# Performance work log

Measured on AMD Instinct MI355X. Metric: run time of the kernel, lower is better.

## Reference

```python
import jax, jax.numpy as jnp
import numpy as np
import math

B, C, H, W = 64, 32, 80, 80
HEADS, HD = 8, 4
L = H * W
INV_PI = 1.0 / math.pi


def _conv2d(x, w, pad):
    return jax.lax.conv_general_dilated(x, w, (1, 1), pad, dimension_numbers=('NCHW', 'OIHW', 'NCHW'))


def _lin_angular(x, qkv_w, proj_w, proj_b, dconv_w):
    # x: (B, L, C) -> softmax-free angular linear attention
    qkv = (x @ qkv_w.T).reshape(B, L, 3, HEADS, HD).transpose(2, 0, 3, 1, 4)
    q, k, v = qkv[0], qkv[1], qkv[2]  # (B, HEADS, L, HD)
    q = q / jnp.linalg.norm(q, axis=-1, keepdims=True)
    k = k / jnp.linalg.norm(k, axis=-1, keepdims=True)
    # depthwise conv over L with kernel (9,1), one channel per head
    dconv_v = jax.lax.conv_general_dilated(v, dconv_w, (1, 1), ((4, 4), (0, 0)),
                                           feature_group_count=HEADS,
                                           dimension_numbers=('NCHW', 'OIHW', 'NCHW'))
    attn = jnp.einsum('bhld,bhle->bhde', k, v)  # (B,H,HD,HD)
    out = 0.5 * v + INV_PI * jnp.einsum('bhld,bhde->bhle', q, attn)
    out = out / jnp.linalg.norm(out, axis=-1, keepdims=True)
    out = out + dconv_v
    out = out.transpose(0, 2, 1, 3).reshape(B, L, C)
    return out @ proj_w.T + proj_b


def _xca(x, qkv_w, temp, proj_w, proj_b):
    # x: (B, L, C) -> cross-covariance (channel) attention
    qkv = (x @ qkv_w.T).reshape(B, L, 3, HEADS, HD).transpose(2, 0, 3, 4, 1)
    q, k, v = qkv[0], qkv[1], qkv[2]  # (B, HEADS, HD, L)
    q = q / jnp.maximum(jnp.linalg.norm(q, axis=-1, keepdims=True), 1e-12)
    k = k / jnp.maximum(jnp.linalg.norm(k, axis=-1, keepdims=True), 1e-12)
    attn = jax.nn.softmax(jnp.einsum('bhdn,bhen->bhde', q, k) * temp, axis=-1)
    out = jnp.einsum('bhde,bhen->bhdn', attn, v)  # (B,H,HD,L)
    out = out.transpose(0, 3, 1, 2).reshape(B, L, C)
    return out @ proj_w.T + proj_b


def _chan_vec(f, wa, ba, wa2, ba2, wm, bm, wm2, bm2):
    # f: (B, C, L) -> (B, C, 1) pooled channel descriptor (avg + max branches)
    avg = f.mean(axis=-1)  # (B, C)
    mx = f.max(axis=-1)    # (B, C)
    a = jax.nn.relu(avg @ wa.T + ba) @ wa2.T + ba2
    m = jax.nn.relu(mx @ wm.T + bm) @ wm2.T + bm2
    return (a + m)[..., None]  # (B, C, 1)


def _spatial_gate(a, c1w, c1b, c2w, c2b):
    # a: (B, C, L) -> (B, 1, L) softmax spatial gate
    am = a.reshape(B, C, H, W)
    pooled = jnp.concatenate([am.mean(axis=1, keepdims=True), am.max(axis=1, keepdims=True)], axis=1)
    y = jax.nn.relu(_conv2d(pooled, c1w, ((1, 1), (1, 1))) + c1b[None, :, None, None])
    y = _conv2d(y, c2w, ((1, 1), (1, 1))) + c2b[None, :, None, None]
    return jax.nn.softmax(y.reshape(B, 1, L), axis=-1)


def _forward(rgb, freq, la_qkv_w, la_proj_w, la_proj_b, la_dconv_w,
             xa_qkv_w, xa_temp, xa_proj_w, xa_proj_b,
             c1s_w, c1s_b, c2s_w, c2s_b,
             avg1_w, avg1_b, max1_w, max1_b, avg2_w, avg2_b, max2_w, max2_b,
             avg11_w, avg11_b, max11_w, max11_b, avg22_w, avg22_b, max22_w, max22_b):
    x1 = rgb.reshape(B, C, L).transpose(0, 2, 1)  # to_3d: (B, L, C)
    la1 = _lin_angular(x1, la_qkv_w, la_proj_w, la_proj_b, la_dconv_w)
    x2 = freq.reshape(B, C, L).transpose(0, 2, 1)
    xa1 = _xca(x2, xa_qkv_w, xa_temp, xa_proj_w, xa_proj_b)
    # CAFM works on flattened (B, C, L)
    f1 = la1.transpose(0, 2, 1)
    f2 = xa1.transpose(0, 2, 1)
    a1 = _chan_vec(f1, avg1_w, avg1_b, avg11_w, avg11_b, max1_w, max1_b, max11_w, max11_b)
    a2 = _chan_vec(f2, avg2_w, avg2_b, avg22_w, avg22_b, max2_w, max2_b, max22_w, max22_b)
    cross = jnp.einsum('bci,bdi->bcd', a1, a2)  # (B, C, C)
    a1f = jnp.einsum('bcd,bdl->bcl', jax.nn.softmax(cross, axis=-1), f1)
    a2f = jnp.einsum('bcd,bdl->bcl', jax.nn.softmax(cross.transpose(0, 2, 1), axis=-1), f2)
    g1 = _spatial_gate(a1f, c1s_w, c1s_b, c2s_w, c2s_b)
    g2 = _spatial_gate(a2f, c1s_w, c1s_b, c2s_w, c2s_b)
    f1 = f1 * g1 + f1
    f2 = f2 * g2 + f2
    # torch: (B,C,L).transpose(0,1) -> (C,B,L); sum; permute(1,2,0) -> (B,L,C); to_4d -> (B,C,H,W)
    # transposes cancel: equivalent to (f1+f2).reshape(B, C, H, W)
    return (f1 + f2).reshape(B, C, H, W)


def setup_inputs() -> dict:
    key = jax.random.key(0)
    ks = iter(jax.random.split(key, 40))
    def rn(shape, s=0.05):
        return jax.random.normal(next(ks), shape, dtype=jnp.float32) * s
    return dict(
        rgb=jax.random.normal(next(ks), (B, C, H, W), dtype=jnp.float32),
        freq=jax.random.normal(next(ks), (B, C, H, W), dtype=jnp.float32),
        la_qkv_w=rn((3 * C, C)), la_proj_w=rn((C, C)), la_proj_b=jnp.zeros((C,), jnp.float32),
        la_dconv_w=rn((HEADS, 1, 9, 1)),
        xa_qkv_w=rn((3 * C, C)), xa_temp=jnp.ones((HEADS, 1, 1), jnp.float32),
        xa_proj_w=rn((C, C)), xa_proj_b=jnp.zeros((C,), jnp.float32),
        c1s_w=rn((1, 2, 3, 3)), c1s_b=jnp.zeros((1,), jnp.float32),
        c2s_w=rn((1, 1, 3, 3)), c2s_b=jnp.zeros((1,), jnp.float32),
        avg1_w=rn((16, C)), avg1_b=jnp.zeros((16,), jnp.float32),
        max1_w=rn((16, C)), max1_b=jnp.zeros((16,), jnp.float32),
        avg2_w=rn((16, C)), avg2_b=jnp.zeros((16,), jnp.float32),
        max2_w=rn((16, C)), max2_b=jnp.zeros((16,), jnp.float32),
        avg11_w=rn((C, 16)), avg11_b=jnp.zeros((C,), jnp.float32),
        max11_w=rn((C, 16)), max11_b=jnp.zeros((C,), jnp.float32),
        avg22_w=rn((C, 16)), avg22_b=jnp.zeros((C,), jnp.float32),
        max22_w=rn((C, 16)), max22_b=jnp.zeros((C,), jnp.float32),
    )


def reference(rgb, freq, la_qkv_w, la_proj_w, la_proj_b, la_dconv_w,
              xa_qkv_w, xa_temp, xa_proj_w, xa_proj_b,
              c1s_w, c1s_b, c2s_w, c2s_b,
              avg1_w, avg1_b, max1_w, max1_b, avg2_w, avg2_b, max2_w, max2_b,
              avg11_w, avg11_b, max11_w, max11_b, avg22_w, avg22_b, max22_w, max22_b):
    return _forward(rgb, freq, la_qkv_w, la_proj_w, la_proj_b, la_dconv_w,
                    xa_qkv_w, xa_temp, xa_proj_w, xa_proj_b,
                    c1s_w, c1s_b, c2s_w, c2s_b,
                    avg1_w, avg1_b, max1_w, max1_b, avg2_w, avg2_b, max2_w, max2_b,
                    avg11_w, avg11_b, max11_w, max11_b, avg22_w, avg22_b, max22_w, max22_b)
```

## Files before the change

kernel.cpp:

```cpp
#include <hip/hip_runtime.h>

#define BN 64
#define CN 32
#define HEADSN 8
#define HDN 4
#define LN 6400
#define CL (CN*LN)


__device__ __forceinline__ unsigned fenc(float f){
  unsigned u = __float_as_uint(f);
  return (u & 0x80000000u) ? ~u : (u | 0x80000000u);
}
__device__ __forceinline__ float fdec(unsigned u){
  unsigned v = (u & 0x80000000u) ? (u & 0x7FFFFFFFu) : ~u;
  return __uint_as_float(v);
}

__device__ __forceinline__ unsigned pk_bf16(float a, float b){
  unsigned ua = __float_as_uint(a), ub = __float_as_uint(b);
  ua = (ua + 0x7fffu + ((ua >> 16) & 1u)) >> 16;
  ub = (ub + 0x7fffu + ((ub >> 16) & 1u)) >> 16;
  return ua | (ub << 16);
}
// ... 163 lines not shown
    if (lane < 32) atomicAdd(la_attn + b*128 + wave*32 + ch, s);
  } else {
    const float* Wq = Wxa + (0  + wave*8)*32;
    const float* Wk = Wxa + (32 + wave*8)*32;
    float acc[48];
    #pragma unroll
    for (int i = 0; i < 48; ++i) acc[i] = 0.f;
    for (int it = 0; it < 2; ++it){
      const int ll = it*64 + lane;
      float xv[32];
      #pragma unroll
      for (int c2 = 0; c2 < 16; ++c2){
        float2 t = xs[ll*17 + c2];
        xv[2*c2] = t.x; xv[2*c2+1] = t.y;
      }
      float qq[8], kk[8];
      #pragma unroll
      for (int r = 0; r < 8; ++r){ qq[r] = 0.f; kk[r] = 0.f; }
      #pragma unroll
      for (int c = 0; c < 32; ++c){
        #pragma unroll
        for (int r = 0; r < 8; ++r){
          qq[r] = fmaf(Wq[r*32 + c], xv[c], qq[r]);
          kk[r] = fmaf(Wk[r*32 + c], xv[c], kk[r]);
        }
      }
      #pragma unroll
      for (int hh = 0; hh < 2; ++hh){
        const float* q = qq + hh*4;
        const float* k = kk + hh*4;
        const int base = hh*24;
        #pragma unroll
        for (int d = 0; d < 4; ++d){
          #pragma unroll
          for (int e = 0; e < 4; ++e)
            acc[base + d*4 + e] = fmaf(q[d], k[e], acc[base + d*4 + e]);
        }
        #pragma unroll
        for (int d = 0; d < 4; ++d) acc[base + 16 + d] = fmaf(q[d], q[d], acc[base + 16 + d]);
        #pragma unroll
        for (int e = 0; e < 4; ++e) acc[base + 20 + e] = fmaf(k[e], k[e], acc[base + 20 + e]);
      }
    }
    float* dst = xa_sums + b*192 + wave*48;
    int ch;
    float s0 = bfly32<false>(acc, lane, &ch);
    if (lane < 32) atomicAdd(dst + ch, s0);
    int ch2;
    float s1 = bfly16_sum(acc + 32, lane, &ch2);
    if (lane < 16) atomicAdd(dst + 32 + ch2, s1);
  }
}

__global__ __launch_bounds__(512) void k_finalize2(const float* __restrict__ rgb,
    const float* __restrict__ freq, const float* __restrict__ Wqkv,
    const float* __restrict__ la_attn, const float* __restrict__ dconv_w,
    const float* __restrict__ Wp, const float* __restrict__ bp,
    const float* __restrict__ Wxa, const float* __restrict__ xtemp,
    const float* __restrict__ xWp, const float* __restrict__ xbp,
    const float* __restrict__ xa_sums,
    float* __restrict__ f1, float* __restrict__ sum1, unsigned* __restrict__ max1e,
    float* __restrict__ f2, float* __restrict__ sum2, unsigned* __restrict__ max2e){
  __shared__ unsigned vsh[2*264*17];
  const bool isXA = blockIdx.x >= 13;
  const int b = blockIdx.y, tid = threadIdx.x;
  const int half = tid >> 8, t = tid & 255;
  const int bxt = isXA ? (int)blockIdx.x - 13 : (int)blockIdx.x;
  const int tile = bxt*2 + half;
  const bool valid = tile < 25;
  const int l0 = tile*256;
  const int l = l0 + t, lane = tid & 63;
  unsigned* vs = vsh + half*(264*17);
  if (!isXA){
    const float* xg = rgb + (size_t)b*CL;
    float x[32];
    if (valid){
      #pragma unroll
      for (int c = 0; c < 32; ++c) x[c] = xg[c*LN + l];
      {
        float v[32];
        #pragma unroll
        for (int r = 0; r < 32; ++r) v[r] = 0.f;
        const float* Wv = Wqkv + 64*32;
        #pragma unroll
        for (int c = 0; c < 32; ++c){
          #pragma unroll
          for (int r = 0; r < 32; ++r) v[r] = fmaf(Wv[r*32 + c], x[c], v[r]);
        }
        #pragma unroll
        for (int c2 = 0; c2 < 16; ++c2)
          vs[(t+4)*17 + c2] = pk_bf16(v[2*c2], v[2*c2+1]);
      }
      if (t < 128){
        const int p = t >> 4, c2 = t & 15;
        const int hl  = (p < 4) ? (l0 - 4 + p) : (l0 + 252 + p);
        const int pos = (p < 4) ? p : (256 + p);
        float2 vh = make_float2(0.f, 0.f);
        if (hl >= 0 && hl < LN){
          const float* W0 = Wqkv + (64 + 2*c2)*32;
          #pragma unroll 8
          for (int cc = 0; cc < 32; ++cc){
            float xv = xg[cc*LN + hl];
            vh.x = fmaf(W0[cc],      xv, vh.x);
            vh.y = fmaf(W0[32 + cc], xv, vh.y);
          }
        }
        vs[pos*17 + c2] = pk_bf16(vh.x, vh.y);
      }
    }
    __syncthreads();
    if (valid){
      float y[32];
      #pragma unroll
      for (int h = 0; h < 8; ++h){
        float q0 = 0.f, q1 = 0.f, q2 = 0.f, q3 = 0.f;
        const float* Wq = Wqkv + h*4*32;
        #pragma unroll
        for (int c = 0; c < 32; ++c){
          q0 = fmaf(Wq[c],      x[c], q0);
          q1 = fmaf(Wq[32 + c], x[c], q1);
          q2 = fmaf(Wq[64 + c], x[c], q2);
          q3 = fmaf(Wq[96 + c], x[c], q3);
        }
        const float rnq = rsqrtf(q0*q0 + q1*q1 + q2*q2 + q3*q3);
        q0 *= rnq; q1 *= rnq; q2 *= rnq; q3 *= rnq;
        const float* at = la_attn + b*128 + h*16;
        const float2 v01 = upk_bf16(vs[(t+4)*17 + h*2]);
        const float2 v23 = upk_bf16(vs[(t+4)*17 + h*2 + 1]);
        const float vo[4] = {v01.x, v01.y, v23.x, v23.y};
        float o[4]; float ss = 0.f;
        #pragma unroll
        for (int e = 0; e < 4; ++e){
          float tt = 0.f;
          tt = fmaf(q0, at[e],      tt);
          tt = fmaf(q1, at[4 + e],  tt);
          tt = fmaf(q2, at[8 + e],  tt);
          tt = fmaf(q3, at[12 + e], tt);
          o[e] = fmaf(0.31830988618379067f, tt, 0.5f*vo[e]);
          ss = fmaf(o[e], o[e], ss);
        }
        const float rno = rsqrtf(ss);
        float dc[4] = {0.f, 0.f, 0.f, 0.f};
        #pragma unroll
        for (int j = 0; j < 9; ++j){
          const float w = dconv_w[h*9 + j];
          const float2 p0 = upk_bf16(vs[(t + j)*17 + h*2]);
          const float2 p1 = upk_bf16(vs[(t + j)*17 + h*2 + 1]);
          dc[0] = fmaf(w, p0.x, dc[0]);
          dc[1] = fmaf(w, p0.y, dc[1]);
          dc[2] = fmaf(w, p1.x, dc[2]);
          dc[3] = fmaf(w, p1.y, dc[3]);
        }
        #pragma unroll
        for (int e = 0; e < 4; ++e) y[h*4 + e] = fmaf(o[e], rno, dc[e]);
      }
      float vals[32];
      float* f1p = f1 + (size_t)b*CL + l;
      #pragma unroll
      for (int r = 0; r < 32; ++r){
        float val = bp[r];
        #pragma unroll
        for (int c = 0; c < 32; ++c) val = fmaf(Wp[r*32 + c], y[c], val);
        f1p[r*LN] = val;
        vals[r] = val;
      }
      int ch;
      float s = bfly32<false>(vals, lane, &ch);
      float m = bfly32<true >(vals, lane, &ch);
      if (lane < 32){
        atomicAdd(&sum1[b*32 + ch], s);
        atomicMax(&max1e[b*32 + ch], fenc(m));
      }
    }
  } else {
    float* M2s    = (float*)vsh;
    float* attn_s = ((float*)vsh) + 1024;
    if (tid < 32){
      const int h = tid >> 2, d = tid & 3;
      const float* xss = xa_sums + b*192 + h*24;
      const float tmp = xtemp[h];
      const float nq = fmaxf(sqrtf(xss[16 + d]), 1e-12f);
      float lg[4]; float m = -1e30f;
      #pragma unroll
      for (int e = 0; e < 4; ++e){
        float nk = fmaxf(sqrtf(xss[20 + e]), 1e-12f);
        lg[e] = xss[d*4 + e] * tmp / (nq*nk);
        m = fmaxf(m, lg[e]);
      }
      float Z = 0.f;
      #pragma unroll
      for (int e = 0; e < 4; ++e){ lg[e] = __expf(lg[e] - m); Z += lg[e]; }
      float iZ = 1.f/Z;
      #pragma unroll
      for (int e = 0; e < 4; ++e) attn_s[h*16 + d*4 + e] = lg[e]*iZ;
    }
    __syncthreads();
    if (tid < 32){
      const int c = tid;
      const float* Wv = Wxa + 64*32;
      float tmpv[32];
      #pragma unroll
      for (int k = 0; k < 32; ++k){
        const int h = k >> 2, d = k & 3;
        float s = 0.f;
        #pragma unroll
        for (int e = 0; e < 4; ++e)
          s = fmaf(attn_s[h*16 + d*4 + e], Wv[(h*4 + e)*32 + c], s);
        tmpv[k] = s;
      }
      float out[32];
      #pragma unroll
      for (int r = 0; r < 32; ++r) out[r] = 0.f;
      #pragma unroll
      for (int k = 0; k < 32; ++k){
        #pragma unroll
        for (int r = 0; r < 32; ++r)
          out[r] = fmaf(xWp[r*32 + k], tmpv[k], out[r]);
      }
      #pragma unroll
      for (int r = 0; r < 32; ++r) M2s[r*32 + c] = out[r];
    }
    __syncthreads();
    if (valid){
      const float* xg = freq + (size_t)b*CL;
      float x[32];
      #pragma unroll
      for (int c = 0; c < 32; ++c) x[c] = xg[c*LN + l];
      float vals[32];
      #pragma unroll
      for (int r = 0; r < 32; ++r) vals[r] = xbp[r];
      #pragma unroll
      for (int c = 0; c < 32; ++c){
        #pragma unroll
        for (int r = 0; r < 32; ++r) vals[r] = fmaf(M2s[r*32 + c], x[c], vals[r]);
      }
      float* f2p = f2 + (size_t)b*CL + l;
      #pragma unroll
      for (int r = 0; r < 32; ++r) f2p[r*LN] = vals[r];
      int ch;
      float s = bfly32<false>(vals, lane, &ch);
      float m = bfly32<true >(vals, lane, &ch);
      if (lane < 32){
        atomicAdd(&sum2[b*32 + ch], s);
        atomicMax(&max2e[b*32 + ch], fenc(m));
      }
    }
  }
}

__global__ __launch_bounds__(256) void k_mix(const float* __restrict__ f1,
    const float* __restrict__ f2,
    const float* __restrict__ sum1, const unsigned* __restrict__ max1e,
    const float* __restrict__ sum2, const unsigned* __restrict__ max2e,
    const float* __restrict__ a1w, const float* __restrict__ a1b,
    const float* __restrict__ m1w, const float* __restrict__ m1b,
    const float* __restrict__ a2w, const float* __restrict__ a2b,
    const float* __restrict__ m2w, const float* __restrict__ m2b,
    const float* __restrict__ a11w, const float* __restrict__ a11b,
    const float* __restrict__ m11w, const float* __restrict__ m11b,
    const float* __restrict__ a22w, const float* __restrict__ a22b,
    const float* __restrict__ m22w, const float* __restrict__ m22b,
    float* __restrict__ pooled1, float* __restrict__ pooled2){
  __shared__ float avg1[32], mx1[32], avg2[32], mx2[32];
  __shared__ float h_a1[16], h_m1[16], h_a2[16], h_m2[16];
  __shared__ float a1v[32], a2v[32];
  __shared__ float w1s[1024], w2s[1024];
  const int b = blockIdx.y, tid = threadIdx.x;
  const int l = blockIdx.x*256 + tid;
  if (tid < 32){
    avg1[tid] = sum1[b*32 + tid] * (1.f/6400.f);
    mx1[tid]  = fdec(max1e[b*32 + tid]);
    avg2[tid] = sum2[b*32 + tid] * (1.f/6400.f);
    mx2[tid]  = fdec(max2e[b*32 + tid]);
  }
  __syncthreads();
  if (tid < 16){
    float s1 = a1b[tid], s2 = m1b[tid], s3 = a2b[tid], s4 = m2b[tid];
    for (int c = 0; c < 32; ++c){
      s1 = fmaf(avg1[c], a1w[tid*32 + c], s1);
      s2 = fmaf(mx1[c],  m1w[tid*32 + c], s2);
      s3 = fmaf(avg2[c], a2w[tid*32 + c], s3);
      s4 = fmaf(mx2[c],  m2w[tid*32 + c], s4);
    }
    h_a1[tid] = fmaxf(s1, 0.f); h_m1[tid] = fmaxf(s2, 0.f);
    h_a2[tid] = fmaxf(s3, 0.f); h_m2[tid] = fmaxf(s4, 0.f);
  }
  __syncthreads();
  if (tid < 32){
    float v1 = a11b[tid] + m11b[tid];
    float v2 = a22b[tid] + m22b[tid];
    for (int k = 0; k < 16; ++k){
      v1 += h_a1[k]*a11w[tid*16 + k] + h_m1[k]*m11w[tid*16 + k];
      v2 += h_a2[k]*a22w[tid*16 + k] + h_m2[k]*m22w[tid*16 + k];
    }
    a1v[tid] = v1; a2v[tid] = v2;
  }
  __syncthreads();
  if (tid < 32){
    float s = a1v[tid], m = -1e30f;
    for (int d = 0; d < 32; ++d) m = fmaxf(m, s*a2v[d]);
    float Z = 0.f;
    for (int d = 0; d < 32; ++d) Z += __expf(s*a2v[d] - m);
    float iZ = 1.f/Z;
    for (int d = 0; d < 32; ++d) w1s[tid*32 + d] = __expf(s*a2v[d] - m)*iZ;
    float s2 = a2v[tid]; m = -1e30f;
    for (int d = 0; d < 32; ++d) m = fmaxf(m, s2*a1v[d]);
    Z = 0.f;
    for (int d = 0; d < 32; ++d) Z += __expf(s2*a1v[d] - m);
    iZ = 1.f/Z;
    for (int d = 0; d < 32; ++d) w2s[tid*32 + d] = __expf(s2*a1v[d] - m)*iZ;
  }
  __syncthreads();
  float fv[32], av[32];
  {
    const float* f1p = f1 + (size_t)b*CL + l;
    #pragma unroll
    for (int d = 0; d < 32; ++d) fv[d] = f1p[d*LN];
    #pragma unroll
    for (int c = 0; c < 32; ++c) av[c] = 0.f;
    #pragma unroll
    for (int d = 0; d < 32; ++d){
      #pragma unroll
      for (int c = 0; c < 32; ++c) av[c] = fmaf(w1s[c*32 + d], fv[d], av[c]);
    }
    float s = 0.f, m = -1e30f;
    #pragma unroll
    for (int c = 0; c < 32; ++c){ s += av[c]; m = fmaxf(m, av[c]); }
    pooled1[(size_t)b*2*LN + l]      = s*(1.f/32.f);
    pooled1[(size_t)b*2*LN + LN + l] = m;
  }
  {
    const float* f2p = f2 + (size_t)b*CL + l;
    #pragma unroll
    for (int d = 0; d < 32; ++d) fv[d] = f2p[d*LN];
    #pragma unroll
    for (int c = 0; c < 32; ++c) av[c] = 0.f;
    #pragma unroll
    for (int d = 0; d < 32; ++d){
      #pragma unroll
      for (int c = 0; c < 32; ++c) av[c] = fmaf(w2s[c*32 + d], fv[d], av[c]);
    }
    float s = 0.f, m = -1e30f;
    #pragma unroll
    for (int c = 0; c < 32; ++c){ s += av[c]; m = fmaxf(m, av[c]); }
    pooled2[(size_t)b*2*LN + l]      = s*(1.f/32.f);
    pooled2[(size_t)b*2*LN + LN + l] = m;
  }
}

__global__ __launch_bounds__(256) void k_gate(const float* __restrict__ pooled1,
    const float* __restrict__ pooled2, const float* __restrict__ c1w,
    const float* __restrict__ c1b, const float* __restrict__ c2w,
    const float* __restrict__ c2b, float* __restrict__ g1, float* __restrict__ g2){
  __shared__ float y1s[6400];
  __shared__ float red[8];
  const int b = blockIdx.y, t = blockIdx.x, tid = threadIdx.x;
  const float* src = (t == 0 ? pooled1 : pooled2) + (size_t)b*2*LN;
  float* dst = (t == 0 ? g1 : g2) + (size_t)b*LN;
  for (int i = tid; i < 6400; i += 256){
    const int yy = i/80, xx = i - yy*80;
    float a = c1b[0];
    #pragma unroll
    for (int ky = 0; ky < 3; ++ky){
      const int y2 = yy + ky - 1;
      if (y2 < 0 || y2 >= 80) continue;
      #pragma unroll
      for (int kx = 0; kx < 3; ++kx){
        const int x2 = xx + kx - 1;
        if (x2 < 0 || x2 >= 80) continue;
        const int j = y2*80 + x2;
        a = fmaf(src[j],        c1w[ky*3 + kx],     a);
        a = fmaf(src[6400 + j], c1w[9 + ky*3 + kx], a);
      }
    }
    y1s[i] = fmaxf(a, 0.f);
  }
  __syncthreads();
  float y2r[25]; float lmax = -1e30f;
  #pragma unroll
  for (int ii = 0; ii < 25; ++ii){
    const int i = tid + ii*256;
    const int yy = i/80, xx = i - yy*80;
    float a = c2b[0];
    #pragma unroll
    for (int ky = 0; ky < 3; ++ky){
      const int y2 = yy + ky - 1;
      if (y2 < 0 || y2 >= 80) continue;
      #pragma unroll
      for (int kx = 0; kx < 3; ++kx){
        const int x2 = xx + kx - 1;
        if (x2 < 0 || x2 >= 80) continue;
        a = fmaf(y1s[y2*80 + x2], c2w[ky*3 + kx], a);
      }
    }
    y2r[ii] = a; lmax = fmaxf(lmax, a);
  }
  #pragma unroll
  for (int off = 32; off >= 1; off >>= 1) lmax = fmaxf(lmax, __shfl_xor(lmax, off, 64));
  if ((tid & 63) == 0) red[tid >> 6] = lmax;
  __syncthreads();
  const float bmax = fmaxf(fmaxf(red[0], red[1]), fmaxf(red[2], red[3]));
  float lsum = 0.f;
  #pragma unroll
  for (int ii = 0; ii < 25; ++ii){
    float e = __expf(y2r[ii] - bmax);
    y2r[ii] = e; lsum += e;
  }
  #pragma unroll
  for (int off = 32; off >= 1; off >>= 1) lsum += __shfl_xor(lsum, off, 64);
  if ((tid & 63) == 0) red[4 + (tid >> 6)] = lsum;
  __syncthreads();
  const float inv = 1.f/(red[4] + red[5] + red[6] + red[7]);
  #pragma unroll
  for (int ii = 0; ii < 25; ++ii) dst[tid + ii*256] = y2r[ii]*inv;
}

__global__ __launch_bounds__(256) void k_final(const float* __restrict__ f1,
    const float* __restrict__ f2, const float* __restrict__ g1,
    const float* __restrict__ g2, float* __restrict__ out){
  const int i = blockIdx.x*256 + threadIdx.x;
  const int flat = i*4;
  const int b = flat / CL;
  const int rem = flat - b*CL;
  const int l = rem % LN;
  const float4 a  = *(const float4*)(f1 + flat);
  const float4 c  = *(const float4*)(f2 + flat);
  const float4 ga = *(const float4*)(g1 + b*LN + l);
  const float4 gc = *(const float4*)(g2 + b*LN + l);
  float4 o;
  o.x = fmaf(a.x, ga.x, a.x) + fmaf(c.x, gc.x, c.x);
  o.y = fmaf(a.y, ga.y, a.y) + fmaf(c.y, gc.y, c.y);
  o.z = fmaf(a.z, ga.z, a.z) + fmaf(c.z, gc.z, c.z);
  o.w = fmaf(a.w, ga.w, a.w) + fmaf(c.w, gc.w, c.w);
  *(float4*)(out + flat) = o;
}

extern "C" void kernel_launch(void* const* d_in, const int* in_sizes, int n_in,
                              void* d_out, int out_size, void* d_ws, size_t ws_size,
                              hipStream_t stream){
  const float* rgb     = (const float*)d_in[0];
  const float* freq    = (const float*)d_in[1];
  const float* la_qkv  = (const float*)d_in[2];
  const float* la_pw   = (const float*)d_in[3];
  const float* la_pb   = (const float*)d_in[4];
  const float* la_dw   = (const float*)d_in[5];
  const float* xa_qkv  = (const float*)d_in[6];
  const float* xa_temp = (const float*)d_in[7];
  const float* xa_pw   = (const float*)d_in[8];
  const float* xa_pb   = (const float*)d_in[9];
  const float* c1w     = (const float*)d_in[10];
  const float* c1b     = (const float*)d_in[11];
  const float* c2w     = (const float*)d_in[12];
  const float* c2b     = (const float*)d_in[13];

  float* ws = (float*)d_ws;
  size_t o = 0;
  float* f1      = ws + o; o += (size_t)BN*CL;
  float* f2      = ws + o; o += (size_t)BN*CL;
  float* la_attn = ws + o; o += BN*128;
  float* xa_sums = ws + o; o += BN*192;
  float* sum1    = ws + o; o += BN*32;
  unsigned* max1e = (unsigned*)(ws + o); o += BN*32;
  float* sum2    = ws + o; o += BN*32;
  unsigned* max2e = (unsigned*)(ws + o); o += BN*32;
  float* pooled1 = ws + o; o += (size_t)BN*2*LN;
  float* pooled2 = ws + o; o += (size_t)BN*2*LN;
  float* g1      = ws + o; o += (size_t)BN*LN;
  float* g2      = ws + o; o += (size_t)BN*LN;

  const size_t nz = (size_t)BN*128 + BN*192 + (size_t)BN*32*4;
  hipMemsetAsync(la_attn, 0, nz*sizeof(float), stream);

  k_reduce2  <<<dim3(50, BN), 512, 0, stream>>>(rgb, freq, la_qkv, xa_qkv, la_attn, xa_sums);
  k_finalize2<<<dim3(26, BN), 512, 0, stream>>>(rgb, freq, la_qkv, la_attn, la_dw,
                                                la_pw, la_pb,
                                                xa_qkv, xa_temp, xa_pw, xa_pb, xa_sums,
                                                f1, sum1, max1e, f2, sum2, max2e);
  k_mix  <<<dim3(25, BN), 256, 0, stream>>>(f1, f2, sum1, max1e, sum2, max2e,
      (const float*)d_in[14], (const float*)d_in[15], (const float*)d_in[16], (const float*)d_in[17],
      (const float*)d_in[18], (const float*)d_in[19], (const float*)d_in[20], (const float*)d_in[21],
      (const float*)d_in[22], (const float*)d_in[23], (const float*)d_in[24], (const float*)d_in[25],
      (const float*)d_in[26], (const float*)d_in[27], (const float*)d_in[28], (const float*)d_in[29],
      pooled1, pooled2);
  k_gate <<<dim3(2, BN), 256, 0, stream>>>(pooled1, pooled2, c1w, c1b, c2w, c2b, g1, g2);
  k_final<<<12800, 256, 0, stream>>>(f1, f2, g1, g2, (float*)d_out);
}
```

Baseline: 529.7 us.

## Merge LA and XCA finalize paths into one 256-thread block per tile

Restructures k_finalize2 so each 256-thread block handles one 256-position tile for both the linear-attention output (f1) and the cross-covariance output (f2), instead of separate half-grids for each branch with two tiles per 512-thread block. This removes the wasted padded tile and the branch-divergent block roles. In exchange every block recomputes the 32x32 XCA projection matrix, and the freq path now runs serially after the LA path within a thread, which raises per-thread work and register pressure.

```diff
diff --git a/kernel.cpp b/kernel.cpp
--- a/kernel.cpp
+++ b/kernel.cpp
@@ -239,7 +239,7 @@
   }
 }
 
-__global__ __launch_bounds__(512) void k_finalize2(const float* __restrict__ rgb,
+__global__ __launch_bounds__(256) void k_finalize2(const float* __restrict__ rgb,
     const float* __restrict__ freq, const float* __restrict__ Wqkv,
     const float* __restrict__ la_attn, const float* __restrict__ dconv_w,
     const float* __restrict__ Wp, const float* __restrict__ bp,
@@ -248,189 +248,176 @@
     const float* __restrict__ xa_sums,
     float* __restrict__ f1, float* __restrict__ sum1, unsigned* __restrict__ max1e,
     float* __restrict__ f2, float* __restrict__ sum2, unsigned* __restrict__ max2e){
-  __shared__ unsigned vsh[2*264*17];
-  const bool isXA = blockIdx.x >= 13;
-  const int b = blockIdx.y, tid = threadIdx.x;
-  const int half = tid >> 8, t = tid & 255;
-  const int bxt = isXA ? (int)blockIdx.x - 13 : (int)blockIdx.x;
-  const int tile = bxt*2 + half;
-  const bool valid = tile < 25;
-  const int l0 = tile*256;
-  const int l = l0 + t, lane = tid & 63;
-  unsigned* vs = vsh + half*(264*17);
-  if (!isXA){
-    const float* xg = rgb + (size_t)b*CL;
-    float x[32];
-    if (valid){
-      #pragma unroll
-      for (int c = 0; c < 32; ++c) x[c] = xg[c*LN + l];
-      {
-        float v[32];
-        #pragma unroll
-        for (int r = 0; r < 32; ++r) v[r] = 0.f;
-        const float* Wv = Wqkv + 64*32;
-        #pragma unroll
-        for (int c = 0; c < 32; ++c){
-          #pragma unroll
-          for (int r = 0; r < 32; ++r) v[r] = fmaf(Wv[r*32 + c], x[c], v[r]);
-        }
-        #pragma unroll
-        for (int c2 = 0; c2 < 16; ++c2)
-          vs[(t+4)*17 + c2] = pk_bf16(v[2*c2], v[2*c2+1]);
-      }
-      if (t < 128){
-        const int p = t >> 4, c2 = t & 15;
-        const int hl  = (p < 4) ? (l0 - 4 + p) : (l0 + 252 + p);
-        const int pos = (p < 4) ? p : (256 + p);
-        float2 vh = make_float2(0.f, 0.f);
-        if (hl >= 0 && hl < LN){
-          const float* W0 = Wqkv + (64 + 2*c2)*32;
-          #pragma unroll 8
-          for (int cc = 0; cc < 32; ++cc){
-            float xv = xg[cc*LN + hl];
-            vh.x = fmaf(W0[cc],      xv, vh.x);
-            vh.y = fmaf(W0[32 + cc], xv, vh.y);
-          }
-        }
-        vs[pos*17 + c2] = pk_bf16(vh.x, vh.y);
-      }
-    }
-    __syncthreads();
-    if (valid){
-      float y[32];
-      #pragma unroll
-      for (int h = 0; h < 8; ++h){
-        float q0 = 0.f, q1 = 0.f, q2 = 0.f, q3 = 0.f;
-        const float* Wq = Wqkv + h*4*32;
-        #pragma unroll
-        for (int c = 0; c < 32; ++c){
-          q0 = fmaf(Wq[c],      x[c], q0);
-          q1 = fmaf(Wq[32 + c], x[c], q1);
-          q2 = fmaf(Wq[64 + c], x[c], q2);
-          q3 = fmaf(Wq[96 + c], x[c], q3);
-        }
-        const float rnq = rsqrtf(q0*q0 + q1*q1 + q2*q2 + q3*q3);
-        q0 *= rnq; q1 *= rnq; q2 *= rnq; q3 *= rnq;
-        const float* at = la_attn + b*128 + h*16;
-        const float2 v01 = upk_bf16(vs[(t+4)*17 + h*2]);
-        const float2 v23 = upk_bf16(vs[(t+4)*17 + h*2 + 1]);
-        const float vo[4] = {v01.x, v01.y, v23.x, v23.y};
-        float o[4]; float ss = 0.f;
-        #pragma unroll
-        for (int e = 0; e < 4; ++e){
-          float tt = 0.f;
-          tt = fmaf(q0, at[e],      tt);
-          tt = fmaf(q1, at[4 + e],  tt);
-          tt = fmaf(q2, at[8 + e],  tt);
-          tt = fmaf(q3, at[12 + e], tt);
-          o[e] = fmaf(0.31830988618379067f, tt, 0.5f*vo[e]);
-          ss = fmaf(o[e], o[e], ss);
-        }
-        const float rno = rsqrtf(ss);
-        float dc[4] = {0.f, 0.f, 0.f, 0.f};
-        #pragma unroll
-        for (int j = 0; j < 9; ++j){
-          const float w = dconv_w[h*9 + j];
-          const float2 p0 = upk_bf16(vs[(t + j)*17 + h*2]);
-          const float2 p1 = upk_bf16(vs[(t + j)*17 + h*2 + 1]);
-          dc[0] = fmaf(w, p0.x, dc[0]);
-          dc[1] = fmaf(w, p0.y, dc[1]);
-          dc[2] = fmaf(w, p1.x, dc[2]);
-          dc[3] = fmaf(w, p1.y, dc[3]);
-        }
-        #pragma unroll
-        for (int e = 0; e < 4; ++e) y[h*4 + e] = fmaf(o[e], rno, dc[e]);
-      }
-      float vals[32];
-      float* f1p = f1 + (size_t)b*CL + l;
-      #pragma unroll
-      for (int r = 0; r < 32; ++r){
-        float val = bp[r];
-        #pragma unroll
-        for (int c = 0; c < 32; ++c) val = fmaf(Wp[r*32 + c], y[c], val);
-        f1p[r*LN] = val;
-        vals[r] = val;
-      }
-      int ch;
-      float s = bfly32<false>(vals, lane, &ch);
-      float m = bfly32<true >(vals, lane, &ch);
-      if (lane < 32){
-        atomicAdd(&sum1[b*32 + ch], s);
-        atomicMax(&max1e[b*32 + ch], fenc(m));
-      }
-    }
-  } else {
-    float* M2s    = (float*)vsh;
-    float* attn_s = ((float*)vsh) + 1024;
-    if (tid < 32){
-      const int h = tid >> 2, d = tid & 3;
-      const float* xss = xa_sums + b*192 + h*24;
-      const float tmp = xtemp[h];
-      const float nq = fmaxf(sqrtf(xss[16 + d]), 1e-12f);
-      float lg[4]; float m = -1e30f;
+  __shared__ unsigned vsh[264*17];
+  __shared__ float M2s[1024];
+  __shared__ float attn_s[128];
+  const int b = blockIdx.y, l0 = blockIdx.x*256, tid = threadIdx.x;
+  const int l = l0 + tid, lane = tid & 63;
+  const float* xg = rgb + (size_t)b*CL;
+  float x[32];
+  #pragma unroll
+  for (int c = 0; c < 32; ++c) x[c] = xg[c*LN + l];
+  {
+    float v[32];
+    #pragma unroll
+    for (int r = 0; r < 32; ++r) v[r] = 0.f;
+    const float* Wv = Wqkv + 64*32;
+    #pragma unroll
+    for (int c = 0; c < 32; ++c){
+      #pragma unroll
+      for (int r = 0; r < 32; ++r) v[r] = fmaf(Wv[r*32 + c], x[c], v[r]);
+    }
+    #pragma unroll
+    for (int c2 = 0; c2 < 16; ++c2)
+      vsh[(tid+4)*17 + c2] = pk_bf16(v[2*c2], v[2*c2+1]);
+  }
+  if (tid < 128){
+    const int p = tid >> 4, c2 = tid & 15;
+    const int hl  = (p < 4) ? (l0 - 4 + p) : (l0 + 252 + p);
+    const int pos = (p < 4) ? p : (256 + p);
+    float2 vh = make_float2(0.f, 0.f);
+    if (hl >= 0 && hl < LN){
+      const float* W0 = Wqkv + (64 + 2*c2)*32;
+      #pragma unroll 8
+      for (int cc = 0; cc < 32; ++cc){
+        float xv = xg[cc*LN + hl];
+        vh.x = fmaf(W0[cc],      xv, vh.x);
+        vh.y = fmaf(W0[32 + cc], xv, vh.y);
+      }
+    }
+    vsh[pos*17 + c2] = pk_bf16(vh.x, vh.y);
+  }
+  if (tid < 32){
+    const int h = tid >> 2, d = tid & 3;
+    const float* xss = xa_sums + b*192 + h*24;
+    const float tmp = xtemp[h];
+    const float nq = fmaxf(sqrtf(xss[16 + d]), 1e-12f);
+    float lg[4]; float m = -1e30f;
+    #pragma unroll
+    for (int e = 0; e < 4; ++e){
+      float nk = fmaxf(sqrtf(xss[20 + e]), 1e-12f);
+      lg[e] = xss[d*4 + e] * tmp / (nq*nk);
+      m = fmaxf(m, lg[e]);
+    }
+    float Z = 0.f;
+    #pragma unroll
+    for (int e = 0; e < 4; ++e){ lg[e] = __expf(lg[e] - m); Z += lg[e]; }
+    float iZ = 1.f/Z;
+    #pragma unroll
+    for (int e = 0; e < 4; ++e) attn_s[h*16 + d*4 + e] = lg[e]*iZ;
+  }
+  __syncthreads();
+  if (tid < 32){
+    const int c = tid;
+    const float* Wv = Wxa + 64*32;
+    float tmpv[32];
+    #pragma unroll
+    for (int k = 0; k < 32; ++k){
+      const int h = k >> 2, d = k & 3;
+      float s = 0.f;
+      #pragma unroll
+      for (int e = 0; e < 4; ++e)
+        s = fmaf(attn_s[h*16 + d*4 + e], Wv[(h*4 + e)*32 + c], s);
+      tmpv[k] = s;
+    }
+    float out[32];
+    #pragma unroll
+    for (int r = 0; r < 32; ++r) out[r] = 0.f;
+    #pragma unroll
+    for (int k = 0; k < 32; ++k){
+      #pragma unroll
+      for (int r = 0; r < 32; ++r)
+        out[r] = fmaf(xWp[r*32 + k], tmpv[k], out[r]);
+    }
+    #pragma unroll
+    for (int r = 0; r < 32; ++r) M2s[r*32 + c] = out[r];
+  }
+  {
+    float y[32];
+    #pragma unroll
+    for (int h = 0; h < 8; ++h){
+      float q0 = 0.f, q1 = 0.f, q2 = 0.f, q3 = 0.f;
+      const float* Wq = Wqkv + h*4*32;
+      #pragma unroll
+      for (int c = 0; c < 32; ++c){
+        q0 = fmaf(Wq[c],      x[c], q0);
+        q1 = fmaf(Wq[32 + c], x[c], q1);
+        q2 = fmaf(Wq[64 + c], x[c], q2);
+        q3 = fmaf(Wq[96 + c], x[c], q3);
+      }
+      const float rnq = rsqrtf(q0*q0 + q1*q1 + q2*q2 + q3*q3);
+      q0 *= rnq; q1 *= rnq; q2 *= rnq; q3 *= rnq;
+      const float* at = la_attn + b*128 + h*16;
+      const float2 v01 = upk_bf16(vsh[(tid+4)*17 + h*2]);
+      const float2 v23 = upk_bf16(vsh[(tid+4)*17 + h*2 + 1]);
+      const float vo[4] = {v01.x, v01.y, v23.x, v23.y};
+      float o[4]; float ss = 0.f;
       #pragma unroll
       for (int e = 0; e < 4; ++e){
-        float nk = fmaxf(sqrtf(xss[20 + e]), 1e-12f);
-        lg[e] = xss[d*4 + e] * tmp / (nq*nk);
-        m = fmaxf(m, lg[e]);
-      }
-      float Z = 0.f;
-      #pragma unroll
-      for (int e = 0; e < 4; ++e){ lg[e] = __expf(lg[e] - m); Z += lg[e]; }
-      float iZ = 1.f/Z;
-      #pragma unroll
-      for (int e = 0; e < 4; ++e) attn_s[h*16 + d*4 + e] = lg[e]*iZ;
-    }
-    __syncthreads();
-    if (tid < 32){
-      const int c = tid;
-      const float* Wv = Wxa + 64*32;
-      float tmpv[32];
-      #pragma unroll
-      for (int k = 0; k < 32; ++k){
-        const int h = k >> 2, d = k & 3;
-        float s = 0.f;
-        #pragma unroll
-        for (int e = 0; e < 4; ++e)
-          s = fmaf(attn_s[h*16 + d*4 + e], Wv[(h*4 + e)*32 + c], s);
-        tmpv[k] = s;
-      }
-      float out[32];
-      #pragma unroll
-      for (int r = 0; r < 32; ++r) out[r] = 0.f;
-      #pragma unroll
-      for (int k = 0; k < 32; ++k){
-        #pragma unroll
-        for (int r = 0; r < 32; ++r)
-          out[r] = fmaf(xWp[r*32 + k], tmpv[k], out[r]);
-      }
-      #pragma unroll
-      for (int r = 0; r < 32; ++r) M2s[r*32 + c] = out[r];
-    }
-    __syncthreads();
-    if (valid){
-      const float* xg = freq + (size_t)b*CL;
-      float x[32];
-      #pragma unroll
-      for (int c = 0; c < 32; ++c) x[c] = xg[c*LN + l];
-      float vals[32];
-      #pragma unroll
-      for (int r = 0; r < 32; ++r) vals[r] = xbp[r];
-      #pragma unroll
-      for (int c = 0; c < 32; ++c){
-        #pragma unroll
-        for (int r = 0; r < 32; ++r) vals[r] = fmaf(M2s[r*32 + c], x[c], vals[r]);
-      }
-      float* f2p = f2 + (size_t)b*CL + l;
-      #pragma unroll
-      for (int r = 0; r < 32; ++r) f2p[r*LN] = vals[r];
-      int ch;
-      float s = bfly32<false>(vals, lane, &ch);
-      float m = bfly32<true >(vals, lane, &ch);
-      if (lane < 32){
-        atomicAdd(&sum2[b*32 + ch], s);
-        atomicMax(&max2e[b*32 + ch], fenc(m));
-      }
+        float t = 0.f;
+        t = fmaf(q0, at[e],      t);
+        t = fmaf(q1, at[4 + e],  t);
+        t = fmaf(q2, at[8 + e],  t);
+        t = fmaf(q3, at[12 + e], t);
+        o[e] = fmaf(0.31830988618379067f, t, 0.5f*vo[e]);
+        ss = fmaf(o[e], o[e], ss);
+      }
+      const float rno = rsqrtf(ss);
+      float dc[4] = {0.f, 0.f, 0.f, 0.f};
+      #pragma unroll
+      for (int j = 0; j < 9; ++j){
+        const float w = dconv_w[h*9 + j];
+        const float2 p0 = upk_bf16(vsh[(tid + j)*17 + h*2]);
+        const float2 p1 = upk_bf16(vsh[(tid + j)*17 + h*2 + 1]);
+        dc[0] = fmaf(w, p0.x, dc[0]);
+        dc[1] = fmaf(w, p0.y, dc[1]);
+        dc[2] = fmaf(w, p1.x, dc[2]);
+        dc[3] = fmaf(w, p1.y, dc[3]);
+      }
+      #pragma unroll
+      for (int e = 0; e < 4; ++e) y[h*4 + e] = fmaf(o[e], rno, dc[e]);
+    }
+    float vals[32];
+    float* f1p = f1 + (size_t)b*CL + l;
+    #pragma unroll
+    for (int r = 0; r < 32; ++r){
+      float val = bp[r];
+      #pragma unroll
+      for (int c = 0; c < 32; ++c) val = fmaf(Wp[r*32 + c], y[c], val);
+      f1p[r*LN] = val;
+      vals[r] = val;
+    }
+    int ch;
+    float s = bfly32<false>(vals, lane, &ch);
+    float m = bfly32<true >(vals, lane, &ch);
+    if (lane < 32){
+      atomicAdd(&sum1[b*32 + ch], s);
+      atomicMax(&max1e[b*32 + ch], fenc(m));
+    }
+  }
+  __syncthreads();
+  {
+    const float* xf = freq + (size_t)b*CL;
+    float xv[32];
+    #pragma unroll
+    for (int c = 0; c < 32; ++c) xv[c] = xf[c*LN + l];
+    float vals[32];
+    #pragma unroll
+    for (int r = 0; r < 32; ++r) vals[r] = xbp[r];
+    #pragma unroll
+    for (int c = 0; c < 32; ++c){
+      #pragma unroll
+      for (int r = 0; r < 32; ++r) vals[r] = fmaf(M2s[r*32 + c], xv[c], vals[r]);
+    }
+    float* f2p = f2 + (size_t)b*CL + l;
+    #pragma unroll
+    for (int r = 0; r < 32; ++r) f2p[r*LN] = vals[r];
+    int ch;
+    float s = bfly32<false>(vals, lane, &ch);
+    float m = bfly32<true >(vals, lane, &ch);
+    if (lane < 32){
+      atomicAdd(&sum2[b*32 + ch], s);
+      atomicMax(&max2e[b*32 + ch], fenc(m));
     }
   }
 }
@@ -659,7 +646,7 @@
   hipMemsetAsync(la_attn, 0, nz*sizeof(float), stream);
 
   k_reduce2  <<<dim3(50, BN), 512, 0, stream>>>(rgb, freq, la_qkv, xa_qkv, la_attn, xa_sums);
-  k_finalize2<<<dim3(26, BN), 512, 0, stream>>>(rgb, freq, la_qkv, la_attn, la_dw,
+  k_finalize2<<<dim3(25, BN), 256, 0, stream>>>(rgb, freq, la_qkv, la_attn, la_dw,
                                                 la_pw, la_pb,
                                                 xa_qkv, xa_temp, xa_pw, xa_pb, xa_sums,
                                                 f1, sum1, max1e, f2, sum2, max2e);
```

Measured after the change: 566.2 us. 6.9% more time.

## Co-schedule LA and XA halves in one block and widen gate kernel

Applied to the files above, without the earlier changes.

Each finalize block now covers one 256-position tile. Its first 256 threads handle the linear-attention path and the other 256 handle the cross-covariance path for the same tile. The per-batch XA matrix setup, which used to run on 32 threads, is spread across all 256 XA threads and interleaved with the LA head loops across barrier phases. This removes the idle padded tile and the serial single-warp prologue. The gate kernel moves from 256 to 1024 threads per block, giving more parallelism to its 128 blocks at the cost of more barrier and reduction overhead.

```diff
diff --git a/kernel.cpp b/kernel.cpp
--- a/kernel.cpp
+++ b/kernel.cpp
@@ -248,122 +248,56 @@
     const float* __restrict__ xa_sums,
     float* __restrict__ f1, float* __restrict__ sum1, unsigned* __restrict__ max1e,
     float* __restrict__ f2, float* __restrict__ sum2, unsigned* __restrict__ max2e){
-  __shared__ unsigned vsh[2*264*17];
-  const bool isXA = blockIdx.x >= 13;
-  const int b = blockIdx.y, tid = threadIdx.x;
-  const int half = tid >> 8, t = tid & 255;
-  const int bxt = isXA ? (int)blockIdx.x - 13 : (int)blockIdx.x;
-  const int tile = bxt*2 + half;
-  const bool valid = tile < 25;
-  const int l0 = tile*256;
+  __shared__ unsigned vsh[264*17];
+  __shared__ float attn_s[128];
+  __shared__ float tmpv_s[1024];
+  __shared__ float M2s[1024];
+  const int b = blockIdx.y, l0 = blockIdx.x*256, tid = threadIdx.x;
+  const bool isLA = tid < 256;
+  const int t = tid & 255;
   const int l = l0 + t, lane = tid & 63;
-  unsigned* vs = vsh + half*(264*17);
-  if (!isXA){
+  float x[32];
+  float y[32];
+  if (isLA){
     const float* xg = rgb + (size_t)b*CL;
-    float x[32];
-    if (valid){
-      #pragma unroll
-      for (int c = 0; c < 32; ++c) x[c] = xg[c*LN + l];
-      {
-        float v[32];
+    #pragma unroll
+    for (int c = 0; c < 32; ++c) x[c] = xg[c*LN + l];
+    {
+      float v[32];
+      #pragma unroll
+      for (int r = 0; r < 32; ++r) v[r] = 0.f;
+      const float* Wv = Wqkv + 64*32;
+      #pragma unroll
+      for (int c = 0; c < 32; ++c){
         #pragma unroll
-        for (int r = 0; r < 32; ++r) v[r] = 0.f;
-        const float* Wv = Wqkv + 64*32;
-        #pragma unroll
-        for (int c = 0; c < 32; ++c){
-          #pragma unroll
-          for (int r = 0; r < 32; ++r) v[r] = fmaf(Wv[r*32 + c], x[c], v[r]);
+        for (int r = 0; r < 32; ++r) v[r] = fmaf(Wv[r*32 + c], x[c], v[r]);
+      }
+      #pragma unroll
+      for (int c2 = 0; c2 < 16; ++c2)
+        vsh[(t+4)*17 + c2] = pk_bf16(v[2*c2], v[2*c2+1]);
+    }
+    if (t < 128){
+      const int p = t >> 4, c2 = t & 15;
+      const int hl  = (p < 4) ? (l0 - 4 + p) : (l0 + 252 + p);
+      const int pos = (p < 4) ? p : (256 + p);
+      float2 vh = make_float2(0.f, 0.f);
+      if (hl >= 0 && hl < LN){
+        const float* W0 = Wqkv + (64 + 2*c2)*32;
+        #pragma unroll 8
+        for (int cc = 0; cc < 32; ++cc){
+          float xv = xg[cc*LN + hl];
+          vh.x = fmaf(W0[cc],      xv, vh.x);
+          vh.y = fmaf(W0[32 + cc], xv, vh.y);
         }
-        #pragma unroll
-        for (int c2 = 0; c2 < 16; ++c2)
-          vs[(t+4)*17 + c2] = pk_bf16(v[2*c2], v[2*c2+1]);
-      }
-      if (t < 128){
-        const int p = t >> 4, c2 = t & 15;
-        const int hl  = (p < 4) ? (l0 - 4 + p) : (l0 + 252 + p);
-        const int pos = (p < 4) ? p : (256 + p);
-        float2 vh = make_float2(0.f, 0.f);
-        if (hl >= 0 && hl < LN){
-          const float* W0 = Wqkv + (64 + 2*c2)*32;
-          #pragma unroll 8
-          for (int cc = 0; cc < 32; ++cc){
-            float xv = xg[cc*LN + hl];
-            vh.x = fmaf(W0[cc],      xv, vh.x);
-            vh.y = fmaf(W0[32 + cc], xv, vh.y);
-          }
-        }
-        vs[pos*17 + c2] = pk_bf16(vh.x, vh.y);
-      }
-    }
-    __syncthreads();
-    if (valid){
-      float y[32];
-      #pragma unroll
-      for (int h = 0; h < 8; ++h){
-        float q0 = 0.f, q1 = 0.f, q2 = 0.f, q3 = 0.f;
-        const float* Wq = Wqkv + h*4*32;
-        #pragma unroll
-        for (int c = 0; c < 32; ++c){
-          q0 = fmaf(Wq[c],      x[c], q0);
-          q1 = fmaf(Wq[32 + c], x[c], q1);
-          q2 = fmaf(Wq[64 + c], x[c], q2);
-          q3 = fmaf(Wq[96 + c], x[c], q3);
-        }
-        const float rnq = rsqrtf(q0*q0 + q1*q1 + q2*q2 + q3*q3);
-        q0 *= rnq; q1 *= rnq; q2 *= rnq; q3 *= rnq;
-        const float* at = la_attn + b*128 + h*16;
-        const float2 v01 = upk_bf16(vs[(t+4)*17 + h*2]);
-        const float2 v23 = upk_bf16(vs[(t+4)*17 + h*2 + 1]);
-        const float vo[4] = {v01.x, v01.y, v23.x, v23.y};
-        float o[4]; float ss = 0.f;
-        #pragma unroll
-        for (int e = 0; e < 4; ++e){
-          float tt = 0.f;
-          tt = fmaf(q0, at[e],      tt);
-          tt = fmaf(q1, at[4 + e],  tt);
-          tt = fmaf(q2, at[8 + e],  tt);
-          tt = fmaf(q3, at[12 + e], tt);
-          o[e] = fmaf(0.31830988618379067f, tt, 0.5f*vo[e]);
-          ss = fmaf(o[e], o[e], ss);
-        }
-        const float rno = rsqrtf(ss);
-        float dc[4] = {0.f, 0.f, 0.f, 0.f};
-        #pragma unroll
-        for (int j = 0; j < 9; ++j){
-          const float w = dconv_w[h*9 + j];
-          const float2 p0 = upk_bf16(vs[(t + j)*17 + h*2]);
-          const float2 p1 = upk_bf16(vs[(t + j)*17 + h*2 + 1]);
-          dc[0] = fmaf(w, p0.x, dc[0]);
-          dc[1] = fmaf(w, p0.y, dc[1]);
-          dc[2] = fmaf(w, p1.x, dc[2]);
-          dc[3] = fmaf(w, p1.y, dc[3]);
-        }
-        #pragma unroll
-        for (int e = 0; e < 4; ++e) y[h*4 + e] = fmaf(o[e], rno, dc[e]);
-      }
-      float vals[32];
-      float* f1p = f1 + (size_t)b*CL + l;
-      #pragma unroll
-      for (int r = 0; r < 32; ++r){
-        float val = bp[r];
-        #pragma unroll
-        for (int c = 0; c < 32; ++c) val = fmaf(Wp[r*32 + c], y[c], val);
-        f1p[r*LN] = val;
-        vals[r] = val;
-      }
-      int ch;
-      float s = bfly32<false>(vals, lane, &ch);
-      float m = bfly32<true >(vals, lane, &ch);
-      if (lane < 32){
-        atomicAdd(&sum1[b*32 + ch], s);
-        atomicMax(&max1e[b*32 + ch], fenc(m));
-      }
+      }
+      vsh[pos*17 + c2] = pk_bf16(vh.x, vh.y);
     }
   } else {
-    float* M2s    = (float*)vsh;
-    float* attn_s = ((float*)vsh) + 1024;
-    if (tid < 32){
-      const int h = tid >> 2, d = tid & 3;
+    const float* xf = freq + (size_t)b*CL;
+    #pragma unroll
+    for (int c = 0; c < 32; ++c) x[c] = xf[c*LN + l];
+    if (t < 32){
+      const int h = t >> 2, d = t & 3;
       const float* xss = xa_sums + b*192 + h*24;
       const float tmp = xtemp[h];
       const float nq = fmaxf(sqrtf(xss[16 + d]), 1e-12f);
@@ -381,56 +315,160 @@
       #pragma unroll
       for (int e = 0; e < 4; ++e) attn_s[h*16 + d*4 + e] = lg[e]*iZ;
     }
-    __syncthreads();
-    if (tid < 32){
-      const int c = tid;
-      const float* Wv = Wxa + 64*32;
-      float tmpv[32];
-      #pragma unroll
-      for (int k = 0; k < 32; ++k){
-        const int h = k >> 2, d = k & 3;
-        float s = 0.f;
-        #pragma unroll
-        for (int e = 0; e < 4; ++e)
-          s = fmaf(attn_s[h*16 + d*4 + e], Wv[(h*4 + e)*32 + c], s);
-        tmpv[k] = s;
-      }
-      float out[32];
-      #pragma unroll
-      for (int r = 0; r < 32; ++r) out[r] = 0.f;
-      #pragma unroll
-      for (int k = 0; k < 32; ++k){
-        #pragma unroll
-        for (int r = 0; r < 32; ++r)
-          out[r] = fmaf(xWp[r*32 + k], tmpv[k], out[r]);
-      }
-      #pragma unroll
-      for (int r = 0; r < 32; ++r) M2s[r*32 + c] = out[r];
-    }
-    __syncthreads();
-    if (valid){
-      const float* xg = freq + (size_t)b*CL;
-      float x[32];
-      #pragma unroll
-      for (int c = 0; c < 32; ++c) x[c] = xg[c*LN + l];
-      float vals[32];
-      #pragma unroll
-      for (int r = 0; r < 32; ++r) vals[r] = xbp[r];
+  }
+  __syncthreads();
+  if (isLA){
+    #pragma unroll
+    for (int h = 0; h < 4; ++h){
+      float q0 = 0.f, q1 = 0.f, q2 = 0.f, q3 = 0.f;
+      const float* Wq = Wqkv + h*4*32;
       #pragma unroll
       for (int c = 0; c < 32; ++c){
-        #pragma unroll
-        for (int r = 0; r < 32; ++r) vals[r] = fmaf(M2s[r*32 + c], x[c], vals[r]);
-      }
-      float* f2p = f2 + (size_t)b*CL + l;
-      #pragma unroll
-      for (int r = 0; r < 32; ++r) f2p[r*LN] = vals[r];
-      int ch;
-      float s = bfly32<false>(vals, lane, &ch);
-      float m = bfly32<true >(vals, lane, &ch);
-      if (lane < 32){
-        atomicAdd(&sum2[b*32 + ch], s);
-        atomicMax(&max2e[b*32 + ch], fenc(m));
-      }
+        q0 = fmaf(Wq[c],      x[c], q0);
+        q1 = fmaf(Wq[32 + c], x[c], q1);
+        q2 = fmaf(Wq[64 + c], x[c], q2);
+        q3 = fmaf(Wq[96 + c], x[c], q3);
+      }
+      const float rnq = rsqrtf(q0*q0 + q1*q1 + q2*q2 + q3*q3);
+      q0 *= rnq; q1 *= rnq; q2 *= rnq; q3 *= rnq;
+      const float* at = la_attn + b*128 + h*16;
+      const float2 v01 = upk_bf16(vsh[(t+4)*17 + h*2]);
+      const float2 v23 = upk_bf16(vsh[(t+4)*17 + h*2 + 1]);
+      const float vo[4] = {v01.x, v01.y, v23.x, v23.y};
+      float o[4]; float ss = 0.f;
+      #pragma unroll
+      for (int e = 0; e < 4; ++e){
+        float tt = 0.f;
+        tt = fmaf(q0, at[e],      tt);
+        tt = fmaf(q1, at[4 + e],  tt);
+        tt = fmaf(q2, at[8 + e],  tt);
+        tt = fmaf(q3, at[12 + e], tt);
+        o[e] = fmaf(0.31830988618379067f, tt, 0.5f*vo[e]);
+        ss = fmaf(o[e], o[e], ss);
+      }
+      const float rno = rsqrtf(ss);
+      float dc[4] = {0.f, 0.f, 0.f, 0.f};
+      #pragma unroll
+      for (int j = 0; j < 9; ++j){
+        const float w = dconv_w[h*9 + j];
+        const float2 p0 = upk_bf16(vsh[(t + j)*17 + h*2]);
+        const float2 p1 = upk_bf16(vsh[(t + j)*17 + h*2 + 1]);
+        dc[0] = fmaf(w, p0.x, dc[0]);
+        dc[1] = fmaf(w, p0.y, dc[1]);
+        dc[2] = fmaf(w, p1.x, dc[2]);
+        dc[3] = fmaf(w, p1.y, dc[3]);
+      }
+      #pragma unroll
+      for (int e = 0; e < 4; ++e) y[h*4 + e] = fmaf(o[e], rno, dc[e]);
+    }
+  } else {
+    const float* Wv = Wxa + 64*32;
+    #pragma unroll
+    for (int i = 0; i < 4; ++i){
+      const int idx = t*4 + i;
+      const int k = idx >> 5, c = idx & 31;
+      const int h = k >> 2, d = k & 3;
+      float s = 0.f;
+      #pragma unroll
+      for (int e = 0; e < 4; ++e)
+        s = fmaf(attn_s[h*16 + d*4 + e], Wv[(h*4 + e)*32 + c], s);
+      tmpv_s[k*32 + c] = s;
+    }
+  }
+  __syncthreads();
+  if (isLA){
+    #pragma unroll
+    for (int h = 4; h < 8; ++h){
+      float q0 = 0.f, q1 = 0.f, q2 = 0.f, q3 = 0.f;
+      const float* Wq = Wqkv + h*4*32;
+      #pragma unroll
+      for (int c = 0; c < 32; ++c){
+        q0 = fmaf(Wq[c],      x[c], q0);
+        q1 = fmaf(Wq[32 + c], x[c], q1);
+        q2 = fmaf(Wq[64 + c], x[c], q2);
+        q3 = fmaf(Wq[96 + c], x[c], q3);
+      }
+      const float rnq = rsqrtf(q0*q0 + q1*q1 + q2*q2 + q3*q3);
+      q0 *= rnq; q1 *= rnq; q2 *= rnq; q3 *= rnq;
+      const float* at = la_attn + b*128 + h*16;
+      const float2 v01 = upk_bf16(vsh[(t+4)*17 + h*2]);
+      const float2 v23 = upk_bf16(vsh[(t+4)*17 + h*2 + 1]);
+      const float vo[4] = {v01.x, v01.y, v23.x, v23.y};
+      float o[4]; float ss = 0.f;
+      #pragma unroll
+      for (int e = 0; e < 4; ++e){
+        float tt = 0.f;
+        tt = fmaf(q0, at[e],      tt);
+        tt = fmaf(q1, at[4 + e],  tt);
+        tt = fmaf(q2, at[8 + e],  tt);
+        tt = fmaf(q3, at[12 + e], tt);
+        o[e] = fmaf(0.31830988618379067f, tt, 0.5f*vo[e]);
+        ss = fmaf(o[e], o[e], ss);
+      }
+      const float rno = rsqrtf(ss);
+      float dc[4] = {0.f, 0.f, 0.f, 0.f};
+      #pragma unroll
+      for (int j = 0; j < 9; ++j){
+        const float w = dconv_w[h*9 + j];
+        const float2 p0 = upk_bf16(vsh[(t + j)*17 + h*2]);
+        const float2 p1 = upk_bf16(vsh[(t + j)*17 + h*2 + 1]);
+        dc[0] = fmaf(w, p0.x, dc[0]);
+        dc[1] = fmaf(w, p0.y, dc[1]);
+        dc[2] = fmaf(w, p1.x, dc[2]);
+        dc[3] = fmaf(w, p1.y, dc[3]);
+      }
+      #pragma unroll
+      for (int e = 0; e < 4; ++e) y[h*4 + e] = fmaf(o[e], rno, dc[e]);
+    }
+  } else {
+    #pragma unroll
+    for (int i = 0; i < 4; ++i){
+      const int idx = t*4 + i;
+      const int r = idx >> 5, c = idx & 31;
+      float s = 0.f;
+      #pragma unroll
+      for (int k = 0; k < 32; ++k)
+        s = fmaf(xWp[r*32 + k], tmpv_s[k*32 + c], s);
+      M2s[r*32 + c] = s;
+    }
+  }
+  __syncthreads();
+  if (isLA){
+    float vals[32];
+    float* f1p = f1 + (size_t)b*CL + l;
+    #pragma unroll
+    for (int r = 0; r < 32; ++r){
+      float val = bp[r];
+      #pragma unroll
+      for (int c = 0; c < 32; ++c) val = fmaf(Wp[r*32 + c], y[c], val);
+      f1p[r*LN] = val;
+      vals[r] = val;
+    }
+    int ch;
+    float s = bfly32<false>(vals, lane, &ch);
+    float m = bfly32<true >(vals, lane, &ch);
+    if (lane < 32){
+      atomicAdd(&sum1[b*32 + ch], s);
+      atomicMax(&max1e[b*32 + ch], fenc(m));
+    }
+  } else {
+    float vals[32];
+    #pragma unroll
+    for (int r = 0; r < 32; ++r) vals[r] = xbp[r];
+    #pragma unroll
+    for (int c = 0; c < 32; ++c){
+      #pragma unroll
+      for (int r = 0; r < 32; ++r) vals[r] = fmaf(M2s[r*32 + c], x[c], vals[r]);
+    }
+    float* f2p = f2 + (size_t)b*CL + l;
+    #pragma unroll
+    for (int r = 0; r < 32; ++r) f2p[r*LN] = vals[r];
+    int ch;
+    float s = bfly32<false>(vals, lane, &ch);
+    float m = bfly32<true >(vals, lane, &ch);
+    if (lane < 32){
+      atomicAdd(&sum2[b*32 + ch], s);
+      atomicMax(&max2e[b*32 + ch], fenc(m));
     }
   }
 }
@@ -535,16 +573,16 @@
   }
 }
 
-__global__ __launch_bounds__(256) void k_gate(const float* __restrict__ pooled1,
+__global__ __launch_bounds__(1024) void k_gate(const float* __restrict__ pooled1,
     const float* __restrict__ pooled2, const float* __restrict__ c1w,
     const float* __restrict__ c1b, const float* __restrict__ c2w,
     const float* __restrict__ c2b, float* __restrict__ g1, float* __restrict__ g2){
   __shared__ float y1s[6400];
-  __shared__ float red[8];
+  __shared__ float red[32];
   const int b = blockIdx.y, t = blockIdx.x, tid = threadIdx.x;
   const float* src = (t == 0 ? pooled1 : pooled2) + (size_t)b*2*LN;
   float* dst = (t == 0 ? g1 : g2) + (size_t)b*LN;
-  for (int i = tid; i < 6400; i += 256){
+  for (int i = tid; i < 6400; i += 1024){
     const int yy = i/80, xx = i - yy*80;
     float a = c1b[0];
     #pragma unroll
@@ -563,43 +601,56 @@
     y1s[i] = fmaxf(a, 0.f);
   }
   __syncthreads();
-  float y2r[25]; float lmax = -1e30f;
-  #pragma unroll
-  for (int ii = 0; ii < 25; ++ii){
-    const int i = tid + ii*256;
-    const int yy = i/80, xx = i - yy*80;
-    float a = c2b[0];
-    #pragma unroll
-    for (int ky = 0; ky < 3; ++ky){
-      const int y2 = yy + ky - 1;
-      if (y2 < 0 || y2 >= 80) continue;
-      #pragma unroll
-      for (int kx = 0; kx < 3; ++kx){
-        const int x2 = xx + kx - 1;
-        if (x2 < 0 || x2 >= 80) continue;
-        a = fmaf(y1s[y2*80 + x2], c2w[ky*3 + kx], a);
-      }
-    }
-    y2r[ii] = a; lmax = fmaxf(lmax, a);
+  float y2r[7]; float lmax = -1e30f;
+  #pragma unroll
+  for (int ii = 0; ii < 7; ++ii){
+    const int i = tid + ii*1024;
+    if (i < 6400){
+      const int yy = i/80, xx = i - yy*80;
+      float a = c2b[0];
+      #pragma unroll
+      for (int ky = 0; ky < 3; ++ky){
+        const int y2 = yy + ky - 1;
+        if (y2 < 0 || y2 >= 80) continue;
+        #pragma unroll
+        for (int kx = 0; kx < 3; ++kx){
+          const int x2 = xx + kx - 1;
+          if (x2 < 0 || x2 >= 80) continue;
+          a = fmaf(y1s[y2*80 + x2], c2w[ky*3 + kx], a);
+        }
+      }
+      y2r[ii] = a; lmax = fmaxf(lmax, a);
+    } else y2r[ii] = -1e30f;
   }
   #pragma unroll
   for (int off = 32; off >= 1; off >>= 1) lmax = fmaxf(lmax, __shfl_xor(lmax, off, 64));
   if ((tid & 63) == 0) red[tid >> 6] = lmax;
   __syncthreads();
-  const float bmax = fmaxf(fmaxf(red[0], red[1]), fmaxf(red[2], red[3]));
+  float bmax = red[0];
+  #pragma unroll
+  for (int i = 1; i < 16; ++i) bmax = fmaxf(bmax, red[i]);
   float lsum = 0.f;
   #pragma unroll
-  for (int ii = 0; ii < 25; ++ii){
-    float e = __expf(y2r[ii] - bmax);
-    y2r[ii] = e; lsum += e;
+  for (int ii = 0; ii < 7; ++ii){
+    const int i = tid + ii*1024;
+    if (i < 6400){
+      float e = __expf(y2r[ii] - bmax);
+      y2r[ii] = e; lsum += e;
+    }
   }
   #pragma unroll
   for (int off = 32; off >= 1; off >>= 1) lsum += __shfl_xor(lsum, off, 64);
-  if ((tid & 63) == 0) red[4 + (tid >> 6)] = lsum;
-  __syncthreads();
-  const float inv = 1.f/(red[4] + red[5] + red[6] + red[7]);
-  #pragma unroll
-  for (int ii = 0; ii < 25; ++ii) dst[tid + ii*256] = y2r[ii]*inv;
+  if ((tid & 63) == 0) red[16 + (tid >> 6)] = lsum;
+  __syncthreads();
+  float tsum = 0.f;
+  #pragma unroll
+  for (int i = 0; i < 16; ++i) tsum += red[16 + i];
+  const float inv = 1.f/tsum;
+  #pragma unroll
+  for (int ii = 0; ii < 7; ++ii){
+    const int i = tid + ii*1024;
+    if (i < 6400) dst[i] = y2r[ii]*inv;
+  }
 }
 
 __global__ __launch_bounds__(256) void k_final(const float* __restrict__ f1,
@@ -659,7 +710,7 @@
   hipMemsetAsync(la_attn, 0, nz*sizeof(float), stream);
 
   k_reduce2  <<<dim3(50, BN), 512, 0, stream>>>(rgb, freq, la_qkv, xa_qkv, la_attn, xa_sums);
-  k_finalize2<<<dim3(26, BN), 512, 0, stream>>>(rgb, freq, la_qkv, la_attn, la_dw,
+  k_finalize2<<<dim3(25, BN), 512, 0, stream>>>(rgb, freq, la_qkv, la_attn, la_dw,
                                                 la_pw, la_pb,
                                                 xa_qkv, xa_temp, xa_pw, xa_pb, xa_sums,
                                                 f1, sum1, max1e, f2, sum2, max2e);
@@ -669,6 +720,6 @@
       (const float*)d_in[22], (const float*)d_in[23], (const float*)d_in[24], (const float*)d_in[25],
       (const float*)d_in[26], (const float*)d_in[27], (const float*)d_in[28], (const float*)d_in[29],
       pooled1, pooled2);
-  k_gate <<<dim3(2, BN), 256, 0, stream>>>(pooled1, pooled2, c1w, c1b, c2w, c2b, g1, g2);
+  k_gate <<<dim3(2, BN), 1024, 0, stream>>>(pooled1, pooled2, c1w, c1b, c2w, c2b, g1, g2);
   k_final<<<12800, 256, 0, stream>>>(f1, f2, g1, g2, (float*)d_out);
 }
```

Result: no change. 532.4 us (+0.5%).
